# Performance work log

Measured on AMD Instinct MI355X. Metric: run time of the kernel, lower is better.

The kernel has to match this reference:

```python
import jax, jax.numpy as jnp
import numpy as np

MUL = 64      # multiplicity of each irrep (64x0e + 64x1o)
B = 8192      # batch / number of nodes
INV_SQRT3 = float(1.0 / np.sqrt(3.0))  # e3nn wigner_3j normalization for (1,1,0),(0,1,1),(1,0,1)
# component normalization: alpha = sqrt(dim_out / fan_in), fan_in = sum over paths of mul_u*mul_v
FAN_IN = 2 * MUL * MUL  # two paths feed each output irrep
ALPHA0 = float(np.sqrt(1.0 / FAN_IN))  # l_out = 0, dim 1
ALPHA1 = float(np.sqrt(3.0 / FAN_IN))  # l_out = 1, dim 3


def setup_inputs() -> dict:
    key = jax.random.key(0)
    kx, k0, k1, k2, k3 = jax.random.split(key, 5)
    x = jax.random.normal(kx, (B, 4 * MUL), dtype=jnp.float32)  # [B, 64*1 + 64*3]
    w000 = jax.random.normal(k0, (MUL, MUL, MUL), dtype=jnp.float32)  # 0e x 0e -> 0e
    w110 = jax.random.normal(k1, (MUL, MUL, MUL), dtype=jnp.float32)  # 1o x 1o -> 0e
    w011 = jax.random.normal(k2, (MUL, MUL, MUL), dtype=jnp.float32)  # 0e x 1o -> 1o
    w101 = jax.random.normal(k3, (MUL, MUL, MUL), dtype=jnp.float32)  # 1o x 0e -> 1o
    return {"x": x, "w000": w000, "w110": w110, "w011": w011, "w101": w101}


def reference(x, w000, w110, w011, w101):
    # split concatenated irrep features: scalars then vectors
    x0 = x[:, :MUL]                          # [B, U]      l=0 (e)
    x1 = x[:, MUL:].reshape(-1, MUL, 3)      # [B, U, 3]   l=1 (o)

    # path (0e,0e)->0e : CG = 1
    p000 = jnp.einsum('uvw,bu,bv->bw', w000, x0, x0)
    # path (1o,1o)->0e : CG[i,j] = delta_ij / sqrt(3)
    p110 = jnp.einsum('uvw,bui,bvi->bw', w110, x1, x1) * INV_SQRT3
    out0 = ALPHA0 * (p000 + p110)            # [B, W]

    # path (0e,1o)->1o : CG[j,k] = delta_jk / sqrt(3)
    p011 = jnp.einsum('uvw,bu,bvk->bwk', w011, x0, x1) * INV_SQRT3
    # path (1o,0e)->1o : CG[i,k] = delta_ik / sqrt(3)
    p101 = jnp.einsum('uvw,buk,bv->bwk', w101, x1, x0) * INV_SQRT3
    out1 = ALPHA1 * (p011 + p101)            # [B, W, 3]

    return jnp.concatenate([out0, out1.reshape(out1.shape[0], MUL * 3)], axis=-1)
```

## Files before the change

kernel.cpp:

```cpp
#include <hip/hip_runtime.h>
#include <hip/hip_bf16.h>
#include <cstdint>

#define BM 32
#define NTHREADS 320
#define WS_TILE 524288
#define BUF_B 24576
#define SMEM_BYTES (3*BUF_B + 4*64*32*4)

typedef __bf16 bf16x8_t __attribute__((ext_vector_type(8)));
typedef float f32x4_t __attribute__((ext_vector_type(4)));

__device__ __forceinline__ void async_ld16(const void* g, void* l) {
  __builtin_amdgcn_global_load_lds((const __attribute__((address_space(1))) unsigned int*)g,
                                   (__attribute__((address_space(3))) unsigned int*)l,
                                   16, 0, 0);
}

#define SYNC_V8() asm volatile("s_waitcnt vmcnt(8) lgkmcnt(0)\n\ts_barrier" ::: "memory")
#define SYNC_V0() asm volatile("s_waitcnt vmcnt(0) lgkmcnt(0)\n\ts_barrier" ::: "memory")

__global__ __launch_bounds__(256) void prep_weights(const float* __restrict__ w000,
                                                    const float* __restrict__ w110,
                                                    const float* __restrict__ w011,
                                                    const float* __restrict__ w101,
                                                    char* __restrict__ ws) {
  const float A0  = 0.011048543456039806f;
  const float A0I = A0 * 0.57735026918962576f;
  int t = blockIdx.x * 256 + threadIdx.x;
  int u = t >> 9, f = (t >> 6) & 7, l = t & 63;
  int n = f >> 1, kf = f & 1;
  int w = 16 * n + (l & 15);
  int vbase = 8 * (l >> 4) + 32 * kf;
  bf16x8_t p0, p1, pc;
#pragma unroll
  for (int j = 0; j < 8; ++j) {
    int v = vbase + j;
    float a = w000[u * 4096 + v * 64 + w] * A0;
    float b = w110[u * 4096 + v * 64 + w] * A0I;
    float d = (w011[u * 4096 + v * 64 + w] + w101[v * 4096 + u * 64 + w]) * A0;
    p0[j] = (__bf16)a;
    p1[j] = (__bf16)b;
    pc[j] = (__bf16)d;
  }
  int off = u * 8192 + f * 1024 + l * 16;
  *(bf16x8_t*)(ws + off) = p0;
  *(bf16x8_t*)(ws + WS_TILE + off) = p1;
  *(bf16x8_t*)(ws + 2 * WS_TILE + off) = pc;
}

__global__ __launch_bounds__(NTHREADS, 1) void tp_main(const float* __restrict__ x,
                                                       const char* __restrict__ ws,
                                                       float* __restrict__ out) {
  extern __shared__ char smem[];
  float* xS = (float*)(smem + 3 * BUF_B);
  const int tid = threadIdx.x;
  const int wave = tid >> 6, lane = tid & 63;
  const int lr = lane & 15, lg = lane >> 4;
  const int b0 = blockIdx.x * BM;
  const int role = wave;
  const int tsel = (role == 0) ? 0 : ((role == 1) ? 1 : 2);

  auto STAGE = [&](int uu, int bufB) {
    if (wave < 3) {
      const char* g = ws + wave * WS_TILE + uu * 8192 + lane * 16;
      char* l = smem + bufB + wave * 8192;
#pragma unroll
      for (int c = 0; c < 8; ++c)
        async_ld16(g + c * 1024, l + c * 1024);
    }
  };

  auto LOADB = [&](bf16x8_t (&bfr)[8], int bufB) {
    const char* wt = smem + bufB + tsel * 8192 + lane * 16;
#pragma unroll
    for (int f = 0; f < 8; ++f)
      bfr[f] = *(const bf16x8_t*)(wt + f * 1024);
  };

  STAGE(0, 0);
  STAGE(1, BUF_B);

  for (int idx = tid; idx < 4 * 64 * 32; idx += NTHREADS) {
    int vec = idx >> 11, rem = idx & 2047;
    int uu = rem >> 5, bb = rem & 31;
    int col = (vec == 0) ? uu : (64 + 3 * uu + (vec - 1));
    xS[idx] = x[(b0 + bb) * 256 + col];
  }

  float xp[3][2][2][8];
  if (role == 1) {
#pragma unroll
    for (int vi = 0; vi < 3; ++vi)
#pragma unroll
      for (int m = 0; m < 2; ++m)
#pragma unroll
        for (int kf = 0; kf < 2; ++kf)
#pragma unroll
          for (int j = 0; j < 8; ++j) {
            int v = 8 * lg + 32 * kf + j;
            xp[vi][m][kf][j] = x[(b0 + 16 * m + lr) * 256 + 64 + 3 * v + vi];
          }
  } else {
    const int vsel = (role == 0) ? 0 : (role - 1);
#pragma unroll
    for (int m = 0; m < 2; ++m)
#pragma unroll
      for (int kf = 0; kf < 2; ++kf)
#pragma unroll
        for (int j = 0; j < 8; ++j) {
          int v = 8 * lg + 32 * kf + j;
          int col = (vsel == 0) ? v : (64 + 3 * v + (vsel - 1));
          xp[0][m][kf][j] = x[(b0 + 16 * m + lr) * 256 + col];
        }
  }

  f32x4_t acc[2][4];
#pragma unroll
  for (int m = 0; m < 2; ++m)
#pragma unroll
    for (int n = 0; n < 4; ++n) {
      f32x4_t z = {0.f, 0.f, 0.f, 0.f};
      acc[m][n] = z;
    }

  auto STEP = [&](bf16x8_t (&bfr)[8], int uu) {
    bf16x8_t afr[2][2];
    if (role == 1) {
      float s0a = xS[1 * 2048 + uu * 32 + lr],      s1a = xS[2 * 2048 + uu * 32 + lr],      s2a = xS[3 * 2048 + uu * 32 + lr];
      float s0b = xS[1 * 2048 + uu * 32 + 16 + lr], s1b = xS[2 * 2048 + uu * 32 + 16 + lr], s2b = xS[3 * 2048 + uu * 32 + 16 + lr];
#pragma unroll
      for (int kf = 0; kf < 2; ++kf)
#pragma unroll
        for (int j = 0; j < 8; ++j) {
          afr[0][kf][j] = (__bf16)(s0a * xp[0][0][kf][j] + s1a * xp[1][0][kf][j] + s2a * xp[2][0][kf][j]);
          afr[1][kf][j] = (__bf16)(s0b * xp[0][1][kf][j] + s1b * xp[1][1][kf][j] + s2b * xp[2][1][kf][j]);
        }
    } else {
      float sa = xS[uu * 32 + lr], sb = xS[uu * 32 + 16 + lr];
#pragma unroll
      for (int kf = 0; kf < 2; ++kf)
#pragma unroll
        for (int j = 0; j < 8; ++j) {
          afr[0][kf][j] = (__bf16)(sa * xp[0][0][kf][j]);
          afr[1][kf][j] = (__bf16)(sb * xp[0][1][kf][j]);
        }
    }
#pragma unroll
    for (int m = 0; m < 2; ++m)
#pragma unroll
      for (int n = 0; n < 4; ++n)
#pragma unroll
        for (int kf = 0; kf < 2; ++kf)
          acc[m][n] = __builtin_amdgcn_mfma_f32_16x16x32_bf16(afr[m][kf], bfr[n * 2 + kf], acc[m][n], 0, 0, 0);
  };

  SYNC_V8();

  bf16x8_t bfr[8];
  for (int base = 0; base < 60; base += 3) {
    STAGE(base + 2, 2 * BUF_B);
    LOADB(bfr, 0);
    STEP(bfr, base);
    SYNC_V8();

    STAGE(base + 3, 0);
    LOADB(bfr, BUF_B);
    STEP(bfr, base + 1);
    SYNC_V8();

    STAGE(base + 4, BUF_B);
    LOADB(bfr, 2 * BUF_B);
    STEP(bfr, base + 2);
    SYNC_V8();
  }
  STAGE(62, 2 * BUF_B);
  LOADB(bfr, 0);
  STEP(bfr, 60);
  SYNC_V8();

  STAGE(63, 0);
  LOADB(bfr, BUF_B);
  STEP(bfr, 61);
  SYNC_V8();

  LOADB(bfr, 2 * BUF_B);
  STEP(bfr, 62);
  SYNC_V0();

  LOADB(bfr, 0);
  STEP(bfr, 63);

  __syncthreads();
  float* pscr = (float*)smem;
  if (role == 1) {
#pragma unroll
    for (int m = 0; m < 2; ++m)
#pragma unroll
      for (int n = 0; n < 4; ++n)
#pragma unroll
        for (int r = 0; r < 4; ++r)
          pscr[(16 * m + 4 * lg + r) * 64 + 16 * n + lr] = acc[m][n][r];
  }
  __syncthreads();
  if (role == 0) {
#pragma unroll
    for (int m = 0; m < 2; ++m)
#pragma unroll
      for (int n = 0; n < 4; ++n)
#pragma unroll
        for (int r = 0; r < 4; ++r) {
          int row = 16 * m + 4 * lg + r, col = 16 * n + lr;
          out[(b0 + row) * 256 + col] = acc[m][n][r] + pscr[row * 64 + col];
        }
  } else if (role >= 2) {
    const int k = role - 2;
#pragma unroll
    for (int m = 0; m < 2; ++m)
#pragma unroll
      for (int n = 0; n < 4; ++n)
#pragma unroll
        for (int r = 0; r < 4; ++r) {
          int row = 16 * m + 4 * lg + r, col = 16 * n + lr;
          out[(b0 + row) * 256 + 64 + 3 * col + k] = acc[m][n][r];
        }
  }
}

extern "C" void kernel_launch(void* const* d_in, const int* in_sizes, int n_in,
                              void* d_out, int out_size, void* d_ws, size_t ws_size,
                              hipStream_t stream) {
  const float* x    = (const float*)d_in[0];
  const float* w000 = (const float*)d_in[1];
  const float* w110 = (const float*)d_in[2];
  const float* w011 = (const float*)d_in[3];
  const float* w101 = (const float*)d_in[4];
  float* out = (float*)d_out;
  char* ws = (char*)d_ws;

  prep_weights<<<128, 256, 0, stream>>>(w000, w110, w011, w101, ws);

  hipFuncSetAttribute((const void*)tp_main, hipFuncAttributeMaxDynamicSharedMemorySize, SMEM_BYTES);
  tp_main<<<256, NTHREADS, SMEM_BYTES, stream>>>(x, ws, out);
}
```

Baseline: 59.74 us.

## Split K dimension across wave pairs to double waves per block

Doubles the block from 5 to 10 waves by splitting each role's K dimension (the two kf halves) across a pair of waves, so each wave issues half the MFMAs and holds half the B/A fragments. Weight staging is spread over 6 waves with 4 async loads each, and the wait count drops from 8 to 4 to match. Partial sums are reduced through shared memory in an extra stage before output. This aims to raise latency hiding and per-CU MFMA issue at the cost of extra reduction traffic and one more barrier.

```diff
diff --git a/kernel.cpp b/kernel.cpp
--- a/kernel.cpp
+++ b/kernel.cpp
@@ -3,7 +3,7 @@
 #include <cstdint>
 
 #define BM 32
-#define NTHREADS 320
+#define NTHREADS 640
 #define WS_TILE 524288
 #define BUF_B 24576
 #define SMEM_BYTES (3*BUF_B + 4*64*32*4)
@@ -17,7 +17,7 @@
                                    16, 0, 0);
 }
 
-#define SYNC_V8() asm volatile("s_waitcnt vmcnt(8) lgkmcnt(0)\n\ts_barrier" ::: "memory")
+#define SYNC_V4() asm volatile("s_waitcnt vmcnt(4) lgkmcnt(0)\n\ts_barrier" ::: "memory")
 #define SYNC_V0() asm volatile("s_waitcnt vmcnt(0) lgkmcnt(0)\n\ts_barrier" ::: "memory")
 
 __global__ __launch_bounds__(256) void prep_weights(const float* __restrict__ w000,
@@ -58,24 +58,25 @@
   const int wave = tid >> 6, lane = tid & 63;
   const int lr = lane & 15, lg = lane >> 4;
   const int b0 = blockIdx.x * BM;
-  const int role = wave;
-  const int tsel = (role == 0) ? 0 : ((role == 1) ? 1 : 2);
+  const int unit = wave >> 1;
+  const int kf = wave & 1;
+  const int tsel = (unit == 0) ? 0 : ((unit == 1) ? 1 : 2);
 
   auto STAGE = [&](int uu, int bufB) {
-    if (wave < 3) {
-      const char* g = ws + wave * WS_TILE + uu * 8192 + lane * 16;
-      char* l = smem + bufB + wave * 8192;
-#pragma unroll
-      for (int c = 0; c < 8; ++c)
+    if (wave < 6) {
+      const char* g = ws + (wave >> 1) * WS_TILE + uu * 8192 + (wave & 1) * 4096 + lane * 16;
+      char* l = smem + bufB + (wave >> 1) * 8192 + (wave & 1) * 4096 + lane * 16;
+#pragma unroll
+      for (int c = 0; c < 4; ++c)
         async_ld16(g + c * 1024, l + c * 1024);
     }
   };
 
-  auto LOADB = [&](bf16x8_t (&bfr)[8], int bufB) {
-    const char* wt = smem + bufB + tsel * 8192 + lane * 16;
-#pragma unroll
-    for (int f = 0; f < 8; ++f)
-      bfr[f] = *(const bf16x8_t*)(wt + f * 1024);
+  auto LOADB = [&](bf16x8_t (&bfr)[4], int bufB) {
+    const char* wt = smem + bufB + tsel * 8192 + kf * 1024 + lane * 16;
+#pragma unroll
+    for (int n = 0; n < 4; ++n)
+      bfr[n] = *(const bf16x8_t*)(wt + n * 2048);
   };
 
   STAGE(0, 0);
@@ -88,31 +89,26 @@
     xS[idx] = x[(b0 + bb) * 256 + col];
   }
 
-  float xp[3][2][2][8];
-  if (role == 1) {
+  float xp[3][2][8];
+  if (unit == 1) {
 #pragma unroll
     for (int vi = 0; vi < 3; ++vi)
 #pragma unroll
       for (int m = 0; m < 2; ++m)
-#pragma unroll
-        for (int kf = 0; kf < 2; ++kf)
-#pragma unroll
-          for (int j = 0; j < 8; ++j) {
-            int v = 8 * lg + 32 * kf + j;
-            xp[vi][m][kf][j] = x[(b0 + 16 * m + lr) * 256 + 64 + 3 * v + vi];
-          }
-  } else {
-    const int vsel = (role == 0) ? 0 : (role - 1);
-#pragma unroll
-    for (int m = 0; m < 2; ++m)
-#pragma unroll
-      for (int kf = 0; kf < 2; ++kf)
 #pragma unroll
         for (int j = 0; j < 8; ++j) {
           int v = 8 * lg + 32 * kf + j;
-          int col = (vsel == 0) ? v : (64 + 3 * v + (vsel - 1));
-          xp[0][m][kf][j] = x[(b0 + 16 * m + lr) * 256 + col];
+          xp[vi][m][j] = x[(b0 + 16 * m + lr) * 256 + 64 + 3 * v + vi];
         }
+  } else {
+#pragma unroll
+    for (int m = 0; m < 2; ++m)
+#pragma unroll
+      for (int j = 0; j < 8; ++j) {
+        int v = 8 * lg + 32 * kf + j;
+        int col = (unit == 0) ? v : (64 + 3 * v + (unit - 2));
+        xp[0][m][j] = x[(b0 + 16 * m + lr) * 256 + col];
+      }
   }
 
   f32x4_t acc[2][4];
@@ -124,65 +120,62 @@
       acc[m][n] = z;
     }
 
-  auto STEP = [&](bf16x8_t (&bfr)[8], int uu) {
-    bf16x8_t afr[2][2];
-    if (role == 1) {
-      float s0a = xS[1 * 2048 + uu * 32 + lr],      s1a = xS[2 * 2048 + uu * 32 + lr],      s2a = xS[3 * 2048 + uu * 32 + lr];
-      float s0b = xS[1 * 2048 + uu * 32 + 16 + lr], s1b = xS[2 * 2048 + uu * 32 + 16 + lr], s2b = xS[3 * 2048 + uu * 32 + 16 + lr];
-#pragma unroll
-      for (int kf = 0; kf < 2; ++kf)
-#pragma unroll
-        for (int j = 0; j < 8; ++j) {
-          afr[0][kf][j] = (__bf16)(s0a * xp[0][0][kf][j] + s1a * xp[1][0][kf][j] + s2a * xp[2][0][kf][j]);
-          afr[1][kf][j] = (__bf16)(s0b * xp[0][1][kf][j] + s1b * xp[1][1][kf][j] + s2b * xp[2][1][kf][j]);
-        }
+  auto STEP = [&](bf16x8_t (&bfr)[4], int uu) {
+    bf16x8_t afr[2];
+    if (unit == 1) {
+#pragma unroll
+      for (int m = 0; m < 2; ++m) {
+        float s0 = xS[1 * 2048 + uu * 32 + 16 * m + lr];
+        float s1 = xS[2 * 2048 + uu * 32 + 16 * m + lr];
+        float s2 = xS[3 * 2048 + uu * 32 + 16 * m + lr];
+#pragma unroll
+        for (int j = 0; j < 8; ++j)
+          afr[m][j] = (__bf16)(s0 * xp[0][m][j] + s1 * xp[1][m][j] + s2 * xp[2][m][j]);
+      }
     } else {
-      float sa = xS[uu * 32 + lr], sb = xS[uu * 32 + 16 + lr];
-#pragma unroll
-      for (int kf = 0; kf < 2; ++kf)
-#pragma unroll
-        for (int j = 0; j < 8; ++j) {
-          afr[0][kf][j] = (__bf16)(sa * xp[0][0][kf][j]);
-          afr[1][kf][j] = (__bf16)(sb * xp[0][1][kf][j]);
-        }
-    }
-#pragma unroll
-    for (int m = 0; m < 2; ++m)
-#pragma unroll
-      for (int n = 0; n < 4; ++n)
-#pragma unroll
-        for (int kf = 0; kf < 2; ++kf)
-          acc[m][n] = __builtin_amdgcn_mfma_f32_16x16x32_bf16(afr[m][kf], bfr[n * 2 + kf], acc[m][n], 0, 0, 0);
+#pragma unroll
+      for (int m = 0; m < 2; ++m) {
+        float s = xS[uu * 32 + 16 * m + lr];
+#pragma unroll
+        for (int j = 0; j < 8; ++j)
+          afr[m][j] = (__bf16)(s * xp[0][m][j]);
+      }
+    }
+#pragma unroll
+    for (int m = 0; m < 2; ++m)
+#pragma unroll
+      for (int n = 0; n < 4; ++n)
+        acc[m][n] = __builtin_amdgcn_mfma_f32_16x16x32_bf16(afr[m], bfr[n], acc[m][n], 0, 0, 0);
   };
 
-  SYNC_V8();
-
-  bf16x8_t bfr[8];
+  SYNC_V4();
+
+  bf16x8_t bfr[4];
   for (int base = 0; base < 60; base += 3) {
     STAGE(base + 2, 2 * BUF_B);
     LOADB(bfr, 0);
     STEP(bfr, base);
-    SYNC_V8();
+    SYNC_V4();
 
     STAGE(base + 3, 0);
     LOADB(bfr, BUF_B);
     STEP(bfr, base + 1);
-    SYNC_V8();
+    SYNC_V4();
 
     STAGE(base + 4, BUF_B);
     LOADB(bfr, 2 * BUF_B);
     STEP(bfr, base + 2);
-    SYNC_V8();
+    SYNC_V4();
   }
   STAGE(62, 2 * BUF_B);
   LOADB(bfr, 0);
   STEP(bfr, 60);
-  SYNC_V8();
+  SYNC_V4();
 
   STAGE(63, 0);
   LOADB(bfr, BUF_B);
   STEP(bfr, 61);
-  SYNC_V8();
+  SYNC_V4();
 
   LOADB(bfr, 2 * BUF_B);
   STEP(bfr, 62);
@@ -193,17 +186,36 @@
 
   __syncthreads();
   float* pscr = (float*)smem;
-  if (role == 1) {
+  if (kf == 1) {
 #pragma unroll
     for (int m = 0; m < 2; ++m)
 #pragma unroll
       for (int n = 0; n < 4; ++n)
 #pragma unroll
         for (int r = 0; r < 4; ++r)
-          pscr[(16 * m + 4 * lg + r) * 64 + 16 * n + lr] = acc[m][n][r];
+          pscr[unit * 2048 + (16 * m + 4 * lg + r) * 64 + 16 * n + lr] = acc[m][n][r];
   }
   __syncthreads();
-  if (role == 0) {
+  if (kf == 0) {
+#pragma unroll
+    for (int m = 0; m < 2; ++m)
+#pragma unroll
+      for (int n = 0; n < 4; ++n)
+#pragma unroll
+        for (int r = 0; r < 4; ++r)
+          acc[m][n][r] += pscr[unit * 2048 + (16 * m + 4 * lg + r) * 64 + 16 * n + lr];
+    if (unit == 1) {
+#pragma unroll
+      for (int m = 0; m < 2; ++m)
+#pragma unroll
+        for (int n = 0; n < 4; ++n)
+#pragma unroll
+          for (int r = 0; r < 4; ++r)
+            pscr[5 * 2048 + (16 * m + 4 * lg + r) * 64 + 16 * n + lr] = acc[m][n][r];
+    }
+  }
+  __syncthreads();
+  if (wave == 0) {
 #pragma unroll
     for (int m = 0; m < 2; ++m)
 #pragma unroll
@@ -211,10 +223,10 @@
 #pragma unroll
         for (int r = 0; r < 4; ++r) {
           int row = 16 * m + 4 * lg + r, col = 16 * n + lr;
-          out[(b0 + row) * 256 + col] = acc[m][n][r] + pscr[row * 64 + col];
+          out[(b0 + row) * 256 + col] = acc[m][n][r] + pscr[5 * 2048 + row * 64 + col];
         }
-  } else if (role >= 2) {
-    const int k = role - 2;
+  } else if (kf == 0 && unit >= 2) {
+    const int k = unit - 2;
 #pragma unroll
     for (int m = 0; m < 2; ++m)
 #pragma unroll
```

Measured after the change: 49.75 us. 1.2x faster.
